# Performance work log

Hardware: AMD Instinct MI355X
Metric: run time of the kernel (lower is better)

The kernel has to match this reference:

```python
import jax, jax.numpy as jnp
import numpy as np

EPS_NORM = 1e-12
EPS_ENT = 1e-12
TEMPERATURE = 0.5
CONTRAST_DENOM = 128.0 * 100.0


def _l2_normalize(x, axis=-1):
    n = jnp.linalg.norm(x, axis=axis, keepdims=True)
    return x / jnp.maximum(n, EPS_NORM)


def setup_inputs() -> dict:
    key0 = jax.random.key(0)
    k1, k2, k3, k4 = jax.random.split(key0, 4)
    B, L, C = 16, 2048, 512
    M = 512
    return {
        "key": jax.random.normal(k1, (B, L, C), dtype=jnp.float32),
        "query": jax.random.normal(k2, (B, L, C), dtype=jnp.float32),
        "keys": jax.random.uniform(k3, (M, C), dtype=jnp.float32),
        "values": jax.random.uniform(k4, (M, C), dtype=jnp.float32),
        "mode": 0,
    }


def reference(key, query, keys, values, mode):
    B, L, C = key.shape
    k = _l2_normalize(key.reshape(-1, C))    # [T, C]
    q = _l2_normalize(query.reshape(-1, C))  # [T, C]

    # --- gatheringLoss ---
    score = jnp.einsum('tc,mc->tm', k, keys)            # [T, M]
    # top-1 of softmax(score) == argmax(score) (softmax is monotone)
    idx = jnp.argmax(score, axis=1)                     # [T]
    nearest_values = values[idx]                        # [T, C]
    gathering_loss = jnp.mean((q - nearest_values) ** 2)

    logits = score / TEMPERATURE                        # [T, M]
    logp = jax.nn.log_softmax(logits, axis=-1)
    gathered = jnp.take_along_axis(logp, idx[:, None], axis=1)  # [T, 1]
    contrast_loss = jnp.sum(gathered) / (-CONTRAST_DENOM)

    # --- read ---
    weights = jax.nn.softmax(score, axis=-1)            # [T, M]
    # EntropyLoss: mean over rows of -sum(w * log(w + eps))
    entropy_loss = jnp.mean(-jnp.sum(weights * jnp.log(weights + EPS_ENT), axis=-1))
    read_query = weights @ values                       # [T, C]

    return (read_query.reshape(B, L, C), entropy_loss, gathering_loss,
            contrast_loss, keys, values)
```

## Files before the change

### kernel.cpp

```cpp
#include <hip/hip_runtime.h>

typedef short short8 __attribute__((ext_vector_type(8)));
typedef float floatx4 __attribute__((ext_vector_type(4)));

#define C_DIM 512
#define KQ_STRIDE 1040
#define ROWS 128

__device__ __forceinline__ unsigned short f2bf(float f) {
    unsigned u = __builtin_bit_cast(unsigned, f);
    u = u + 0x7fffu + ((u >> 16) & 1u);
    return (unsigned short)(u >> 16);
}

__device__ __forceinline__ unsigned skey(float s, int col) {
    unsigned u = __builtin_bit_cast(unsigned, s);
    u = ((int)u < 0) ? ~u : (u | 0x80000000u);
    return (u & ~0x1FFu) | (unsigned)(511 - col);
}

template <int CTRL>
__device__ __forceinline__ float dppAddF(float x) {
    int t = __builtin_amdgcn_update_dpp(0, __builtin_bit_cast(int, x), CTRL, 0xF, 0xF, true);
    return x + __builtin_bit_cast(float, t);
}
template <int CTRL>
__device__ __forceinline__ unsigned dppMaxU(unsigned x) {
    unsigned u = (unsigned)__builtin_amdgcn_update_dpp(0, (int)x, CTRL, 0xF, 0xF, true);
    return u > x ? u : x;
}
__device__ __forceinline__ float rowAdd16(float x) {
    x = dppAddF<0xB1>(x);
    x = dppAddF<0x4E>(x);
    x = dppAddF<0x124>(x);
    x = dppAddF<0x128>(x);
    return x;
}

__global__ __launch_bounds__(256) void pack_kernel(
    const float* __restrict__ keys, const float* __restrict__ values,
    unsigned short* __restrict__ keysFrag, unsigned short* __restrict__ valsFrag,
    float* __restrict__ keysOut, float* __restrict__ valsOut,
    float* __restrict__ scal) {
    int tid = blockIdx.x * 256 + threadIdx.x;
    if (tid < 65536) {
        int e  = tid & 32767;
        int l  = e & 63;
        int NT = (e >> 6) & 31;
        int kt = e >> 11;
        int li = l & 15, q4 = l >> 4;
        unsigned short tmp[8];
        if (tid < 32768) {
            const float* s = keys + (size_t)(NT * 16 + li) * C_DIM + kt * 32 + q4 * 8;
#pragma unroll
            for (int j = 0; j < 8; j++) tmp[j] = f2bf(s[j]);
            unsigned short* d = keysFrag + ((size_t)(kt * 32 + NT) * 64 + l) * 8;
            *(ushort4*)d       = make_ushort4(tmp[0], tmp[1], tmp[2], tmp[3]);
            *(ushort4*)(d + 4) = make_ushort4(tmp[4], tmp[5], tmp[6], tmp[7]);
        } else {
#pragma unroll
            for (int j = 0; j < 8; j++)
                tmp[j] = f2bf(values[(size_t)(kt * 32 + q4 * 8 + j) * C_DIM + NT * 16 + li]);
            unsigned short* d = valsFrag + ((size_t)(kt * 32 + NT) * 64 + l) * 8;
            *(ushort4*)d       = make_ushort4(tmp[0], tmp[1], tmp[2], tmp[3]);
            *(ushort4*)(d + 4) = make_ushort4(tmp[4], tmp[5], tmp[6], tmp[7]);
        }
    } else {
        int ct = tid - 65536;
        if (ct == 0) { scal[0] = 0.f; scal[1] = 0.f; scal[2] = 0.f; }
#pragma unroll
        for (int i = 0; i < 4; i++) {
            int idx = ct + i * 32768;
            if (idx < 65536) ((float4*)keysOut)[idx] = ((const float4*)keys)[idx];
            else             ((float4*)valsOut)[idx - 65536] = ((const float4*)values)[idx - 65536];
        }
    }
}

__global__ __launch_bounds__(512, 2) void score_kernel(
    const float* __restrict__ key,
    const unsigned short* __restrict__ keysFrag,
    float* __restrict__ outRQ,
    float* __restrict__ scal) {
    __shared__ char kq[ROWS * KQ_STRIDE];
    __shared__ __align__(16) float stats[8][ROWS][4];
    __shared__ float invsh[ROWS];

    const int tid = threadIdx.x;
    const int w  = tid >> 6;
    const int l  = tid & 63;
    const int li = l & 15;
    const int q4 = l >> 4;
    const int row0 = blockIdx.x << 7;
    char* outb = (char*)outRQ;

    const int sr = tid >> 2, sq = tid & 3;
    const float4* krow = (const float4*)(key + (size_t)(row0 + sr) * C_DIM);
    char* sdst = kq + sr * KQ_STRIDE + sq * 32;

    floatx4 acc1[32];
#pragma unroll
    for (int i = 0; i < 32; i++) acc1[i] = (floatx4){0.f, 0.f, 0.f, 0.f};

    const short8* kf = (const short8*)keysFrag;
    short8 bcur[4], bnxt[4];
#pragma unroll
    for (int nt = 0; nt < 4; nt++) bcur[nt] = kf[(size_t)((w * 4 + nt) * 64 + l)];

    float4 va[4], vb[4];
#pragma unroll
    for (int j = 0; j < 4; j++) va[j] = krow[sq * 4 + j];
    float ss = 0.f;

    for (int c = 0; c < 8; ++c) {
        if (c < 7) {
#pragma unroll
            for (int j = 0; j < 4; j++) vb[j] = krow[(c + 1) * 16 + sq * 4 + j];
        }
#pragma unroll
        for (int j = 0; j < 4; j++)
            ss += va[j].x * va[j].x + va[j].y * va[j].y + va[j].z * va[j].z + va[j].w * va[j].w;
        *(ushort4*)(sdst + c * 128) =
            make_ushort4(f2bf(va[0].x), f2bf(va[0].y), f2bf(va[0].z), f2bf(va[0].w));
        *(ushort4*)(sdst + c * 128 + 8) =
            make_ushort4(f2bf(va[1].x), f2bf(va[1].y), f2bf(va[1].z), f2bf(va[1].w));
        *(ushort4*)(sdst + c * 128 + 16) =
            make_ushort4(f2bf(va[2].x), f2bf(va[2].y), f2bf(va[2].z), f2bf(va[2].w));
        *(ushort4*)(sdst + c * 128 + 24) =
            make_ushort4(f2bf(va[3].x), f2bf(va[3].y), f2bf(va[3].z), f2bf(va[3].w));
        __syncthreads();
#pragma unroll
        for (int k2 = 0; k2 < 2; ++k2) {
            int kt = c * 2 + k2;
            if (kt < 15) {
#pragma unroll
                for (int nt = 0; nt < 4; nt++)
                    bnxt[nt] = kf[(size_t)(((kt + 1) * 32 + w * 4 + nt) * 64 + l)];
            }
#pragma unroll
            for (int rg = 0; rg < 8; ++rg) {
                short8 a = *(const short8*)(kq + (rg * 16 + li) * KQ_STRIDE + kt * 64 + q4 * 16);
#pragma unroll
                for (int nt = 0; nt < 4; nt++)
                    acc1[rg * 4 + nt] = __builtin_amdgcn_mfma_f32_16x16x32_bf16(
                        a, bcur[nt], acc1[rg * 4 + nt], 0, 0, 0);
            }
#pragma unroll
            for (int nt = 0; nt < 4; nt++) bcur[nt] = bnxt[nt];
        }
#pragma unroll
        for (int j = 0; j < 4; j++) va[j] = vb[j];
    }

    ss = dppAddF<0xB1>(ss);
    ss = dppAddF<0x4E>(ss);
    if (sq == 0) invsh[sr] = 1.0f / fmaxf(sqrtf(ss), 1e-12f);
    __syncthreads();

#pragma unroll
    for (int rg = 0; rg < 8; rg++) {
#pragma unroll
        for (int reg = 0; reg < 4; reg++) {
            const int colbase = (w << 6) + li;
            const float inv = invsh[rg * 16 + q4 * 4 + reg];
            float s0 = acc1[rg * 4 + 0][reg] * inv;
            float s1 = acc1[rg * 4 + 1][reg] * inv;
            float s2 = acc1[rg * 4 + 2][reg] * inv;
            float s3 = acc1[rg * 4 + 3][reg] * inv;
            unsigned K  = skey(s0, colbase);
            unsigned K1 = skey(s1, colbase + 16);
            unsigned K2 = skey(s2, colbase + 32);
            unsigned K3 = skey(s3, colbase + 48);
            K = K1 > K ? K1 : K;
            K = K2 > K ? K2 : K;
            K = K3 > K ? K3 : K;
            float p0 = __expf(s0), p1 = __expf(s1), p2 = __expf(s2), p3 = __expf(s3);
            float z1 = (p0 + p1) + (p2 + p3);
            float e1 = p0 * s0 + p1 * s1 + p2 * s2 + p3 * s3;
            float z2 = p0 * p0 + p1 * p1 + p2 * p2 + p3 * p3;
            acc1[rg * 4 + 0][reg] = p0;
            acc1[rg * 4 + 1][reg] = p1;
            acc1[rg * 4 + 2][reg] = p2;
            acc1[rg * 4 + 3][reg] = p3;
            K = dppMaxU<0xB1>(K);  z1 = dppAddF<0xB1>(z1);  e1 = dppAddF<0xB1>(e1);  z2 = dppAddF<0xB1>(z2);
            K = dppMaxU<0x4E>(K);  z1 = dppAddF<0x4E>(z1);  e1 = dppAddF<0x4E>(e1);  z2 = dppAddF<0x4E>(z2);
            K = dppMaxU<0x124>(K); z1 = dppAddF<0x124>(z1); e1 = dppAddF<0x124>(e1); z2 = dppAddF<0x124>(z2);
            K = dppMaxU<0x128>(K); z1 = dppAddF<0x128>(z1); e1 = dppAddF<0x128>(e1); z2 = dppAddF<0x128>(z2);
            if (li == 0) {
                floatx4 sv;
                sv[0] = __builtin_bit_cast(float, K);
                sv[1] = z1; sv[2] = e1; sv[3] = z2;
                *(floatx4*)stats[w][rg * 16 + q4 * 4 + reg] = sv;
            }
        }
    }
    __syncthreads();

    if (w == 0) {
        unsigned KA, KB; float z1A, e1A, z2A, z1B, e1B, z2B;
        floatx4 vA = *(const floatx4*)stats[0][l];
        floatx4 vB = *(const floatx4*)stats[0][64 + l];
        KA = __builtin_bit_cast(unsigned, vA[0]); z1A = vA[1]; e1A = vA[2]; z2A = vA[3];
        KB = __builtin_bit_cast(unsigned, vB[0]); z1B = vB[1]; e1B = vB[2]; z2B = vB[3];
#pragma unroll
        for (int p = 1; p < 8; p++) {
            floatx4 uA = *(const floatx4*)stats[p][l];
            floatx4 uB = *(const floatx4*)stats[p][64 + l];
            unsigned KoA = __builtin_bit_cast(unsigned, uA[0]);
            unsigned KoB = __builtin_bit_cast(unsigned, uB[0]);
            KA = KoA > KA ? KoA : KA; z1A += uA[1]; e1A += uA[2]; z2A += uA[3];
            KB = KoB > KB ? KoB : KB; z1B += uB[1]; e1B += uB[2]; z2B += uB[3];
        }
        float izA = 1.0f / z1A, izB = 1.0f / z1B;
        int idxA = 511 - (int)(KA & 0x1FFu);
        int idxB = 511 - (int)(KB & 0x1FFu);
        char* h0 = outb + (size_t)(row0 + l) * 2048;
        char* h1 = outb + (size_t)(row0 + 64 + l) * 2048;
        *(float*)h0 = izA; *(int*)(h0 + 4) = idxA;
        *(float*)h1 = izB; *(int*)(h1 + 4) = idxB;
        unsigned umA = (KA >> 31) ? (KA & 0x7FFFFFFFu) : ~KA;
        unsigned umB = (KB >> 31) ? (KB & 0x7FFFFFFFu) : ~KB;
        umA &= ~0x1FFu; umB &= ~0x1FFu;
        float m1A = __builtin_bit_cast(float, umA);
        float m1B = __builtin_bit_cast(float, umB);
        float ent = (__logf(z1A) - e1A * izA) + (__logf(z1B) - e1B * izB);
        float con = (__logf(z2A) - 2.0f * m1A) + (__logf(z2B) - 2.0f * m1B);
#pragma unroll
        for (int msk = 1; msk < 64; msk <<= 1) {
            ent += __shfl_xor(ent, msk, 64);
            con += __shfl_xor(con, msk, 64);
        }
        if (l == 0) {
            atomicAdd(&scal[0], ent * (1.0f / 32768.0f));
            atomicAdd(&scal[2], con * (1.0f / 12800.0f));
        }
    }

#pragma unroll
    for (int rg = 0; rg < 8; rg++) {
#pragma unroll
        for (int reg = 0; reg < 4; reg++) {
            int r = rg * 16 + q4 * 4 + reg;
#pragma unroll
            for (int nt = 0; nt < 4; nt++) {
                int col = (w << 6) + nt * 16 + li;
                *(unsigned short*)(kq + r * KQ_STRIDE + col * 2) = f2bf(acc1[rg * 4 + nt][reg]);
            }
        }
    }
    __syncthreads();

#pragma unroll
    for (int it = 0; it < 16; it++) {
        int r = (w << 4) + it;
        float4 t = *(const float4*)(kq + r * KQ_STRIDE + l * 16);
        *(float4*)(outb + (size_t)(row0 + r) * 2048 + 1024 + l * 16) = t;
    }
}

__global__ __launch_bounds__(512, 2) void pv_kernel(
    const unsigned short* __restrict__ valsFrag,
    const float* __restrict__ query,
    const float* __restrict__ values,
    float* __restrict__ outRQ,
    float* __restrict__ scal) {
    __shared__ char kq[ROWS * KQ_STRIDE];
    __shared__ float izsh[ROWS];
    __shared__ int   idxsh[ROWS];
    __shared__ float gpart[8];

    const int tid = threadIdx.x;
    const int w  = tid >> 6;
    const int l  = tid & 63;
    const int li = l & 15;
    const int q4 = l >> 4;
    const int row0 = blockIdx.x << 7;
    char* outb = (char*)outRQ;

    const float* qtb = query + (size_t)row0 * C_DIM;
    float tch0 = qtb[(tid)        * 32];
    float tch1 = qtb[(tid +  512) * 32];
    float tch2 = qtb[(tid + 1024) * 32];
    float tch3 = qtb[(tid + 1536) * 32];

    if (tid < ROWS) {
        izsh[tid]  = *(const float*)(outb + (size_t)(row0 + tid) * 2048);
        idxsh[tid] = *(const int*)(outb + (size_t)(row0 + tid) * 2048 + 4);
    }

    const int sr = tid >> 2, sq = tid & 3;
    const char* psrc = outb + (size_t)(row0 + sr) * 2048 + 1024 + sq * 32;
    char* pdst = kq + sr * KQ_STRIDE + sq * 32;

    floatx4 acc2[32];
#pragma unroll
    for (int i = 0; i < 32; i++) acc2[i] = (floatx4){0.f, 0.f, 0.f, 0.f};

    const short8* vf = (const short8*)valsFrag;
    short8 bcur[4], bnxt[4];
#pragma unroll
    for (int nt = 0; nt < 4; nt++) bcur[nt] = vf[(size_t)((w * 4 + nt) * 64 + l)];

    float4 va0 = *(const float4*)(psrc);
    float4 va1 = *(const float4*)(psrc + 16);
    float4 vb0, vb1;

    for (int c = 0; c < 8; ++c) {
        if (c < 7) {
            vb0 = *(const float4*)(psrc + (c + 1) * 128);
            vb1 = *(const float4*)(psrc + (c + 1) * 128 + 16);
        }
        *(float4*)(pdst + c * 128)      = va0;
        *(float4*)(pdst + c * 128 + 16) = va1;
        __syncthreads();
#pragma unroll
        for (int k2 = 0; k2 < 2; ++k2) {
            int kt = c * 2 + k2;
            if (kt < 15) {
#pragma unroll
                for (int nt = 0; nt < 4; nt++)
                    bnxt[nt] = vf[(size_t)(((kt + 1) * 32 + w * 4 + nt) * 64 + l)];
            }
#pragma unroll
            for (int rg = 0; rg < 8; ++rg) {
                short8 a = *(const short8*)(kq + (rg * 16 + li) * KQ_STRIDE + kt * 64 + q4 * 16);
#pragma unroll
                for (int nt = 0; nt < 4; nt++)
                    acc2[rg * 4 + nt] = __builtin_amdgcn_mfma_f32_16x16x32_bf16(
                        a, bcur[nt], acc2[rg * 4 + nt], 0, 0, 0);
            }
#pragma unroll
            for (int nt = 0; nt < 4; nt++) bcur[nt] = bnxt[nt];
        }
        va0 = vb0; va1 = vb1;
    }
    asm volatile("" :: "v"(tch0), "v"(tch1), "v"(tch2), "v"(tch3));

#pragma unroll
    for (int rg = 0; rg < 8; rg++) {
#pragma unroll
        for (int reg = 0; reg < 4; reg++) {
            int r = rg * 16 + q4 * 4 + reg;
            float izr = izsh[r];
            float* orow = outRQ + (size_t)(row0 + r) * C_DIM + (w << 6) + li;
#pragma unroll
            for (int nt = 0; nt < 4; nt++) orow[nt * 16] = acc2[rg * 4 + nt][reg] * izr;
        }
    }

    float gacc = 0.f;
#pragma unroll
    for (int rr = 0; rr < 16; rr++) {
        int r = (w << 4) + rr;
        int idxr = idxsh[r];
        const float4* qr = (const float4*)(query + (size_t)(row0 + r) * C_DIM);
        float4 a = qr[l * 2], b = qr[l * 2 + 1];
        float ss = a.x * a.x + a.y * a.y + a.z * a.z + a.w * a.w +
                   b.x * b.x + b.y * b.y + b.z * b.z + b.w * b.w;
        ss = rowAdd16(ss);
        ss += __shfl_xor(ss, 16, 64);
        ss += __shfl_xor(ss, 32, 64);
        float inv = 1.0f / fmaxf(sqrtf(ss), 1e-12f);
        const float4* vr = (const float4*)(values + (size_t)idxr * C_DIM);
        float4 va = vr[l * 2], vb = vr[l * 2 + 1];
        float d;
        d = a.x * inv - va.x; gacc += d * d;
        d = a.y * inv - va.y; gacc += d * d;
        d = a.z * inv - va.z; gacc += d * d;
        d = a.w * inv - va.w; gacc += d * d;
        d = b.x * inv - vb.x; gacc += d * d;
        d = b.y * inv - vb.y; gacc += d * d;
        d = b.z * inv - vb.z; gacc += d * d;
        d = b.w * inv - vb.w; gacc += d * d;
    }
    gacc = rowAdd16(gacc);
    gacc += __shfl_xor(gacc, 16, 64);
    gacc += __shfl_xor(gacc, 32, 64);
    if (l == 0) gpart[w] = gacc;
    __syncthreads();
    if (tid == 0) {
        float s = 0.f;
#pragma unroll
        for (int i = 0; i < 8; i++) s += gpart[i];
        atomicAdd(&scal[1], s * (1.0f / (32768.0f * 512.0f)));
    }
}

extern "C" void kernel_launch(void* const* d_in, const int* in_sizes, int n_in,
                              void* d_out, int out_size, void* d_ws, size_t ws_size,
                              hipStream_t stream) {
    (void)in_sizes; (void)n_in; (void)out_size; (void)ws_size;
    const float* key    = (const float*)d_in[0];
    const float* query  = (const float*)d_in[1];
    const float* keysIn = (const float*)d_in[2];
    const float* valsIn = (const float*)d_in[3];
    float* out = (float*)d_out;

    unsigned short* keysFrag = (unsigned short*)d_ws;
    unsigned short* valsFrag = keysFrag + 512 * 512;

    float* outRQ   = out;
    float* scal    = out + 16777216;
    float* keysOut = out + 16777219;
    float* valsOut = keysOut + 262144;

    pack_kernel<<<384, 256, 0, stream>>>(keysIn, valsIn, keysFrag, valsFrag,
                                         keysOut, valsOut, scal);
    score_kernel<<<256, 512, 0, stream>>>(key, keysFrag, outRQ, scal);
    pv_kernel<<<256, 512, 0, stream>>>(valsFrag, query, valsIn, outRQ, scal);
}
```

Measured before the change: 237.7 us.

## Split gathering-loss computation out of PV kernel into separate wide-grid kernel

Moves the query normalization and gathering-loss reduction out of the PV matmul kernel into its own kernel launched over 1024 blocks of 256 threads before the PV kernel. The PV kernel loses its query prefetch and serial tail loop, which should shorten its per-block critical path and spread the memory-bound gather across more blocks. The cost is an extra kernel launch, and the gather must finish reading the index slots in the output buffer before the PV kernel overwrites them.

```diff
diff --git a/kernel.cpp b/kernel.cpp
--- a/kernel.cpp
+++ b/kernel.cpp
@@ -258,102 +258,24 @@
     }
 }
 
-__global__ __launch_bounds__(512, 2) void pv_kernel(
-    const unsigned short* __restrict__ valsFrag,
+__global__ __launch_bounds__(256) void gather_kernel(
     const float* __restrict__ query,
     const float* __restrict__ values,
-    float* __restrict__ outRQ,
+    const float* __restrict__ outRQ,
     float* __restrict__ scal) {
-    __shared__ char kq[ROWS * KQ_STRIDE];
-    __shared__ float izsh[ROWS];
-    __shared__ int   idxsh[ROWS];
-    __shared__ float gpart[8];
-
+    __shared__ float gpart[4];
     const int tid = threadIdx.x;
-    const int w  = tid >> 6;
-    const int l  = tid & 63;
-    const int li = l & 15;
-    const int q4 = l >> 4;
-    const int row0 = blockIdx.x << 7;
-    char* outb = (char*)outRQ;
-
-    const float* qtb = query + (size_t)row0 * C_DIM;
-    float tch0 = qtb[(tid)        * 32];
-    float tch1 = qtb[(tid +  512) * 32];
-    float tch2 = qtb[(tid + 1024) * 32];
-    float tch3 = qtb[(tid + 1536) * 32];
-
-    if (tid < ROWS) {
-        izsh[tid]  = *(const float*)(outb + (size_t)(row0 + tid) * 2048);
-        idxsh[tid] = *(const int*)(outb + (size_t)(row0 + tid) * 2048 + 4);
-    }
-
-    const int sr = tid >> 2, sq = tid & 3;
-    const char* psrc = outb + (size_t)(row0 + sr) * 2048 + 1024 + sq * 32;
-    char* pdst = kq + sr * KQ_STRIDE + sq * 32;
-
-    floatx4 acc2[32];
-#pragma unroll
-    for (int i = 0; i < 32; i++) acc2[i] = (floatx4){0.f, 0.f, 0.f, 0.f};
-
-    const short8* vf = (const short8*)valsFrag;
-    short8 bcur[4], bnxt[4];
-#pragma unroll
-    for (int nt = 0; nt < 4; nt++) bcur[nt] = vf[(size_t)((w * 4 + nt) * 64 + l)];
-
-    float4 va0 = *(const float4*)(psrc);
-    float4 va1 = *(const float4*)(psrc + 16);
-    float4 vb0, vb1;
-
-    for (int c = 0; c < 8; ++c) {
-        if (c < 7) {
-            vb0 = *(const float4*)(psrc + (c + 1) * 128);
-            vb1 = *(const float4*)(psrc + (c + 1) * 128 + 16);
-        }
-        *(float4*)(pdst + c * 128)      = va0;
-        *(float4*)(pdst + c * 128 + 16) = va1;
-        __syncthreads();
-#pragma unroll
-        for (int k2 = 0; k2 < 2; ++k2) {
-            int kt = c * 2 + k2;
-            if (kt < 15) {
-#pragma unroll
-                for (int nt = 0; nt < 4; nt++)
-                    bnxt[nt] = vf[(size_t)(((kt + 1) * 32 + w * 4 + nt) * 64 + l)];
-            }
-#pragma unroll
-            for (int rg = 0; rg < 8; ++rg) {
-                short8 a = *(const short8*)(kq + (rg * 16 + li) * KQ_STRIDE + kt * 64 + q4 * 16);
-#pragma unroll
-                for (int nt = 0; nt < 4; nt++)
-                    acc2[rg * 4 + nt] = __builtin_amdgcn_mfma_f32_16x16x32_bf16(
-                        a, bcur[nt], acc2[rg * 4 + nt], 0, 0, 0);
-            }
-#pragma unroll
-            for (int nt = 0; nt < 4; nt++) bcur[nt] = bnxt[nt];
-        }
-        va0 = vb0; va1 = vb1;
-    }
-    asm volatile("" :: "v"(tch0), "v"(tch1), "v"(tch2), "v"(tch3));
-
-#pragma unroll
-    for (int rg = 0; rg < 8; rg++) {
-#pragma unroll
-        for (int reg = 0; reg < 4; reg++) {
-            int r = rg * 16 + q4 * 4 + reg;
-            float izr = izsh[r];
-            float* orow = outRQ + (size_t)(row0 + r) * C_DIM + (w << 6) + li;
-#pragma unroll
-            for (int nt = 0; nt < 4; nt++) orow[nt * 16] = acc2[rg * 4 + nt][reg] * izr;
-        }
-    }
+    const int w = tid >> 6;
+    const int l = tid & 63;
+    const char* outb = (const char*)outRQ;
+    const int row0 = blockIdx.x * 32;
 
     float gacc = 0.f;
 #pragma unroll
-    for (int rr = 0; rr < 16; rr++) {
-        int r = (w << 4) + rr;
-        int idxr = idxsh[r];
-        const float4* qr = (const float4*)(query + (size_t)(row0 + r) * C_DIM);
+    for (int rr = 0; rr < 8; rr++) {
+        int r = row0 + w * 8 + rr;
+        int idxr = *(const int*)(outb + (size_t)r * 2048 + 4);
+        const float4* qr = (const float4*)(query + (size_t)r * C_DIM);
         float4 a = qr[l * 2], b = qr[l * 2 + 1];
         float ss = a.x * a.x + a.y * a.y + a.z * a.z + a.w * a.w +
                    b.x * b.x + b.y * b.y + b.z * b.z + b.w * b.w;
@@ -379,10 +301,84 @@
     if (l == 0) gpart[w] = gacc;
     __syncthreads();
     if (tid == 0) {
-        float s = 0.f;
-#pragma unroll
-        for (int i = 0; i < 8; i++) s += gpart[i];
+        float s = gpart[0] + gpart[1] + gpart[2] + gpart[3];
         atomicAdd(&scal[1], s * (1.0f / (32768.0f * 512.0f)));
+    }
+}
+
+__global__ __launch_bounds__(512, 2) void pv_kernel(
+    const unsigned short* __restrict__ valsFrag,
+    float* __restrict__ outRQ) {
+    __shared__ char kq[ROWS * KQ_STRIDE];
+    __shared__ float izsh[ROWS];
+
+    const int tid = threadIdx.x;
+    const int w  = tid >> 6;
+    const int l  = tid & 63;
+    const int li = l & 15;
+    const int q4 = l >> 4;
+    const int row0 = blockIdx.x << 7;
+    char* outb = (char*)outRQ;
+
+    if (tid < ROWS) izsh[tid] = *(const float*)(outb + (size_t)(row0 + tid) * 2048);
+
+    const int sr = tid >> 2, sq = tid & 3;
+    const char* psrc = outb + (size_t)(row0 + sr) * 2048 + 1024 + sq * 32;
+    char* pdst = kq + sr * KQ_STRIDE + sq * 32;
+
+    floatx4 acc2[32];
+#pragma unroll
+    for (int i = 0; i < 32; i++) acc2[i] = (floatx4){0.f, 0.f, 0.f, 0.f};
+
+    const short8* vf = (const short8*)valsFrag;
+    short8 bcur[4], bnxt[4];
+#pragma unroll
+    for (int nt = 0; nt < 4; nt++) bcur[nt] = vf[(size_t)((w * 4 + nt) * 64 + l)];
+
+    float4 va0 = *(const float4*)(psrc);
+    float4 va1 = *(const float4*)(psrc + 16);
+    float4 vb0, vb1;
+
+    for (int c = 0; c < 8; ++c) {
+        if (c < 7) {
+            vb0 = *(const float4*)(psrc + (c + 1) * 128);
+            vb1 = *(const float4*)(psrc + (c + 1) * 128 + 16);
+        }
+        *(float4*)(pdst + c * 128)      = va0;
+        *(float4*)(pdst + c * 128 + 16) = va1;
+        __syncthreads();
+#pragma unroll
+        for (int k2 = 0; k2 < 2; ++k2) {
+            int kt = c * 2 + k2;
+            if (kt < 15) {
+#pragma unroll
+                for (int nt = 0; nt < 4; nt++)
+                    bnxt[nt] = vf[(size_t)(((kt + 1) * 32 + w * 4 + nt) * 64 + l)];
+            }
+#pragma unroll
+            for (int rg = 0; rg < 8; ++rg) {
+                short8 a = *(const short8*)(kq + (rg * 16 + li) * KQ_STRIDE + kt * 64 + q4 * 16);
+#pragma unroll
+                for (int nt = 0; nt < 4; nt++)
+                    acc2[rg * 4 + nt] = __builtin_amdgcn_mfma_f32_16x16x32_bf16(
+                        a, bcur[nt], acc2[rg * 4 + nt], 0, 0, 0);
+            }
+#pragma unroll
+            for (int nt = 0; nt < 4; nt++) bcur[nt] = bnxt[nt];
+        }
+        va0 = vb0; va1 = vb1;
+    }
+
+#pragma unroll
+    for (int rg = 0; rg < 8; rg++) {
+#pragma unroll
+        for (int reg = 0; reg < 4; reg++) {
+            int r = rg * 16 + q4 * 4 + reg;
+            float izr = izsh[r];
+            float* orow = outRQ + (size_t)(row0 + r) * C_DIM + (w << 6) + li;
+#pragma unroll
+            for (int nt = 0; nt < 4; nt++) orow[nt * 16] = acc2[rg * 4 + nt][reg] * izr;
+        }
     }
 }
 
@@ -407,5 +403,6 @@
     pack_kernel<<<384, 256, 0, stream>>>(keysIn, valsIn, keysFrag, valsFrag,
                                          keysOut, valsOut, scal);
     score_kernel<<<256, 512, 0, stream>>>(key, keysFrag, outRQ, scal);
-    pv_kernel<<<256, 512, 0, stream>>>(valsFrag, query, valsIn, outRQ, scal);
-}
+    gather_kernel<<<1024, 256, 0, stream>>>(query, valsIn, outRQ, scal);
+    pv_kernel<<<256, 512, 0, stream>>>(valsFrag, outRQ);
+}
```

After: 227.3 us. 4.4% less time.
